# Performance work log

Measured on AMD Instinct MI355X. Metric: run time of the kernel, lower is better.

The kernel has to match this reference:

```python
import jax, jax.numpy as jnp
import numpy as np

WINDOW = (2, 7, 7)
SHIFT = (1, 3, 3)
HEADS = 4


def _rel_pos_index(ws):
    coords = np.stack(np.meshgrid(*[np.arange(w) for w in ws], indexing='ij'))  # (3, wd, wh, ww)
    cf = coords.reshape(3, -1)
    rel = cf[:, :, None] - cf[:, None, :]  # (3, N, N)
    rel = rel.transpose(1, 2, 0).astype(np.int64)
    rel[:, :, 0] += ws[0] - 1
    rel[:, :, 1] += ws[1] - 1
    rel[:, :, 2] += ws[2] - 1
    rel[:, :, 0] *= (2 * ws[1] - 1) * (2 * ws[2] - 1)
    rel[:, :, 1] *= 2 * ws[2] - 1
    return rel.sum(-1)  # (N, N)


def _attn_mask(D, H, W, ws, ss):
    img = np.zeros((1, D, H, W, 1), np.float32)
    cnt = 0
    for d in (slice(None, -ws[0]), slice(-ws[0], -ss[0]), slice(-ss[0], None)):
        for h in (slice(None, -ws[1]), slice(-ws[1], -ss[1]), slice(-ss[1], None)):
            for w in (slice(None, -ws[2]), slice(-ws[2], -ss[2]), slice(-ss[2], None)):
                img[:, d, h, w, :] = cnt
                cnt += 1
    N = ws[0] * ws[1] * ws[2]
    mw = img.reshape(1, D // ws[0], ws[0], H // ws[1], ws[1], W // ws[2], ws[2], 1)
    mw = mw.transpose(0, 1, 3, 5, 2, 4, 6, 7).reshape(-1, N)  # (nW, N)
    diff = mw[:, None, :] - mw[:, :, None]
    return np.where(diff != 0, -100.0, 0.0).astype(np.float32)  # (nW, N, N)


def _win_partition(x, ws):
    B, D, H, W, C = x.shape
    x = x.reshape(B, D // ws[0], ws[0], H // ws[1], ws[1], W // ws[2], ws[2], C)
    return x.transpose(0, 1, 3, 5, 2, 4, 6, 7).reshape(-1, ws[0] * ws[1] * ws[2], C)


def _win_reverse(win, ws, B, D, H, W):
    C = win.shape[-1]
    x = win.reshape(B, D // ws[0], H // ws[1], W // ws[2], ws[0], ws[1], ws[2], C)
    return x.transpose(0, 1, 4, 2, 5, 3, 6, 7).reshape(B, D, H, W, C)


def _ln(x, w, b):
    mu = x.mean(-1, keepdims=True)
    var = x.var(-1, keepdims=True)
    return (x - mu) / jnp.sqrt(var + 1e-5) * w + b


def setup_inputs() -> dict:
    key = jax.random.key(0)
    ks = jax.random.split(key, 8)
    B, D, H, W, C = 4, 8, 56, 56, 128
    hidden = 4 * C
    table = (2 * WINDOW[0] - 1) * (2 * WINDOW[1] - 1) * (2 * WINDOW[2] - 1)
    return {
        'x': jax.random.normal(ks[0], (B, D, H, W, C), jnp.float32),
        'norm1_w': jnp.ones((C,), jnp.float32),
        'norm1_b': jnp.zeros((C,), jnp.float32),
        'qkv_w': 0.02 * jax.random.normal(ks[1], (3 * C, C), jnp.float32),
        'qkv_b': jnp.zeros((3 * C,), jnp.float32),
        'rpb': 0.02 * jax.random.normal(ks[2], (table, HEADS), jnp.float32),
        'proj_w': 0.02 * jax.random.normal(ks[3], (C, C), jnp.float32),
        'proj_b': jnp.zeros((C,), jnp.float32),
        'norm2_w': jnp.ones((C,), jnp.float32),
        'norm2_b': jnp.zeros((C,), jnp.float32),
        'fc1_w': 0.02 * jax.random.normal(ks[4], (hidden, C), jnp.float32),
        'fc1_b': jnp.zeros((hidden,), jnp.float32),
        'fc2_w': 0.02 * jax.random.normal(ks[5], (C, hidden), jnp.float32),
        'fc2_b': jnp.zeros((C,), jnp.float32),
    }


def reference(x, norm1_w, norm1_b, qkv_w, qkv_b, rpb, proj_w, proj_b,
              norm2_w, norm2_b, fc1_w, fc1_b, fc2_w, fc2_b):
    B, D, H, W, C = x.shape
    hd = C // HEADS
    scale = hd ** -0.5
    N = WINDOW[0] * WINDOW[1] * WINDOW[2]

    shortcut = x
    y = _ln(x, norm1_w, norm1_b)
    # cyclic shift (SW-MSA)
    y = jnp.roll(y, (-SHIFT[0], -SHIFT[1], -SHIFT[2]), axis=(1, 2, 3))
    win = _win_partition(y, WINDOW)  # (B_, N, C)
    B_ = win.shape[0]

    qkv = win @ qkv_w.T + qkv_b  # (B_, N, 3C)
    qkv = qkv.reshape(B_, N, 3, HEADS, hd).transpose(2, 0, 3, 1, 4)
    q, k, v = qkv[0] * scale, qkv[1], qkv[2]  # (B_, h, N, hd)

    attn = jnp.einsum('bhnd,bhmd->bhnm', q, k)  # (B_, h, N, N)
    rpi = _rel_pos_index(WINDOW)
    bias = rpb[rpi.reshape(-1)].reshape(N, N, HEADS).transpose(2, 0, 1)  # (h, N, N)
    attn = attn + bias[None]

    mask = jnp.asarray(_attn_mask(D, H, W, WINDOW, SHIFT))  # (nW, N, N)
    nW = mask.shape[0]
    attn = attn.reshape(B_ // nW, nW, HEADS, N, N) + mask[None, :, None]
    attn = jax.nn.softmax(attn.reshape(B_, HEADS, N, N), axis=-1)

    out = jnp.einsum('bhnm,bhmd->bhnd', attn, v)
    out = out.transpose(0, 2, 1, 3).reshape(B_, N, C)
    out = out @ proj_w.T + proj_b

    y = _win_reverse(out, WINDOW, B, D, H, W)
    y = jnp.roll(y, SHIFT, axis=(1, 2, 3))  # reverse cyclic shift
    x = shortcut + y

    h = _ln(x, norm2_w, norm2_b)
    h = jax.nn.gelu(h @ fc1_w.T + fc1_b, approximate=False)
    h = h @ fc2_w.T + fc2_b
    return x + h
```

## Files before the change

kernel.cpp:

```cpp
#include <hip/hip_runtime.h>
#include <math.h>

typedef short bf16x8 __attribute__((ext_vector_type(8)));
typedef float f32x4 __attribute__((ext_vector_type(4)));
typedef unsigned short u16;

#define DEVFN static __device__ __forceinline__

DEVFN u16 f2bf(float f) {
  union { float f; unsigned u; } v; v.f = f;
  return (u16)((v.u + 0x7FFFu + ((v.u >> 16) & 1u)) >> 16);
}

DEVFN float bf2f(u16 u) {
  union { unsigned u; float f; } v; v.u = ((unsigned)u) << 16;
  return v.f;
}

DEVFN void gload16(const void* g, void* l) {
  __builtin_amdgcn_global_load_lds(
      (const __attribute__((address_space(1))) void*)g,
      (__attribute__((address_space(3))) void*)l, 16, 0, 0);
}

DEVFN float gelu_fast(float x) {
  float e = __expf(-1.702f * x);
  return x * __builtin_amdgcn_rcpf(1.0f + e);
}

#define TT 100352
#define BWIN 1024

__global__ void convert4_kernel(const float* __restrict__ a, const float* __restrict__ b,
                                const float* __restrict__ c, const float* __restrict__ d,
                                u16* __restrict__ oa, u16* __restrict__ ob,
                                u16* __restrict__ oc, u16* __restrict__ od) {
  int i = blockIdx.x * 256 + threadIdx.x;
  const float* s; u16* o; int off;
  if (i < 49152)       { s = a; o = oa; off = i; }
  else if (i < 65536)  { s = b; o = ob; off = i - 49152; }
  else if (i < 131072) { s = c; o = oc; off = i - 65536; }
  else                 { s = d; o = od; off = i - 131072; }
  o[off] = f2bf(s[off]);
}

__global__ void biasmask_kernel(const float* __restrict__ rpb, float* __restrict__ bm) {
  int idx = blockIdx.x * 256 + threadIdx.x;
  int lane = idx & 63;
  int rem = idx >> 6;
  int nt = rem % 7;  rem /= 7;
  int mt = rem % 7;  rem /= 7;
  int h = rem & 3;
  int pat = rem >> 2;
  int dB = (pat >> 2) & 1, hB = (pat >> 1) & 1, wB = pat & 1;
  int jc = nt * 16 + (lane & 15);
  f32x4 out;
  #pragma unroll
  for (int r = 0; r < 4; ++r) {
    int ic = mt * 16 + (lane >> 4) * 4 + r;
    float v;
    if (jc > 97) v = -30000.f;
    else if (ic > 97) v = 0.f;
    else {
      int di = ic / 49, ri = ic % 49, hi = ri / 7, wi = ri % 7;
      int dj = jc / 49, rj = jc % 49, hj = rj / 7, wj = rj % 7;
      int tidx = (di - dj + 1) * 169 + (hi - hj + 6) * 13 + (wi - wj + 6);
      v = rpb[tidx * 4 + h];
      int ridi = (dB ? (di == 0 ? 1 : 2) * 9 : 0) + (hB ? (hi < 4 ? 1 : 2) * 3 : 0)
               + (wB ? (wi < 4 ? 1 : 2) : 0);
      int ridj = (dB ? (dj == 0 ? 1 : 2) * 9 : 0) + (hB ? (hj < 4 ? 1 : 2) * 3 : 0)
               + (wB ? (wj < 4 ? 1 : 2) : 0);
      if (ridi != ridj) v -= 100.f;
    }
    out[r] = v;
  }
  *(f32x4*)(bm + (size_t)idx * 4) = out;
}

__global__ __launch_bounds__(256) void qkv_kernel(
    const float* __restrict__ x, const float* __restrict__ n1w, const float* __restrict__ n1b,
    const u16* __restrict__ Bw, const float* __restrict__ bias, u16* __restrict__ outp)
{
  __shared__ u16 smem[24576];
  u16* As = smem;
  u16* Bs = smem + 16384;
  const int m0 = blockIdx.x * 128, n0 = blockIdx.y * 128;
  const int t = threadIdx.x;
  const int wid = t >> 6, lane = t & 63;
  const int wr = wid >> 1, wc = wid & 1;
  const int l15 = lane & 15, lhi = lane >> 4;
  const int srow = lane >> 3;
  const int sslot = lane & 7;
  const int gcol = ((sslot ^ srow) << 3);

  {
    const int rowl = t >> 1, half = t & 1;
    const int grow = m0 + rowl;
    int b_ = grow / 98, n = grow % 98;
    int bb = b_ >> 8, widx = b_ & 255;
    int dwv = widx >> 6, hwv = (widx >> 3) & 7, wwv = widx & 7;
    int dd = n / 49, rr = n % 49, hh = rr / 7, wn = rr % 7;
    int d = (dwv * 2 + dd + 1) & 7;
    int hq = hwv * 7 + hh + 3; if (hq >= 56) hq -= 56;
    int wq = wwv * 7 + wn + 3; if (wq >= 56) wq -= 56;
    size_t src = ((size_t)(((bb * 8 + d) * 56 + hq) * 56 + wq)) * 128 + half * 64;
    f32x4 vals[16];
    float s = 0.f, sq = 0.f;
    #pragma unroll
    for (int j = 0; j < 16; ++j) {
      f32x4 v = *(const f32x4*)(x + src + j * 4);
      vals[j] = v;
      s += v[0] + v[1] + v[2] + v[3];
      sq += v[0]*v[0] + v[1]*v[1] + v[2]*v[2] + v[3]*v[3];
    }
    s += __shfl_xor(s, 1, 64);  sq += __shfl_xor(sq, 1, 64);
    float mu = s * (1.0f / 128.0f);
    float var = sq * (1.0f / 128.0f) - mu * mu;
    float rstd = rsqrtf(var + 1e-5f);
    #pragma unroll
    for (int j = 0; j < 8; ++j) {
      int col = half * 64 + j * 8;
      f32x4 wv0 = *(const f32x4*)(n1w + col);
      f32x4 wv1 = *(const f32x4*)(n1w + col + 4);
      f32x4 bv0 = *(const f32x4*)(n1b + col);
      f32x4 bv1 = *(const f32x4*)(n1b + col + 4);
      u16 hb[8];
      #pragma unroll
      for (int e = 0; e < 4; ++e) {
        hb[e]     = f2bf((vals[2*j][e]   - mu) * rstd * wv0[e] + bv0[e]);
        hb[e + 4] = f2bf((vals[2*j+1][e] - mu) * rstd * wv1[e] + bv1[e]);
      }
      *(bf16x8*)(As + rowl * 128 + ((((col >> 3) ^ (rowl & 7))) << 3)) = *(const bf16x8*)hb;
    }
  }

  f32x4 acc[4][4] = {};
  for (int k0 = 0; k0 < 128; k0 += 64) {
    #pragma unroll
    for (int it = 0; it < 4; ++it) {
      const int rbase = it * 32 + wid * 8;
      const int row = rbase + srow;
      gload16(Bw + (size_t)(n0 + row) * 128 + k0 + gcol, Bs + rbase * 64);
    }
    __syncthreads();
    #pragma unroll
    for (int kk = 0; kk < 64; kk += 32) {
      bf16x8 af[4], bfr[4];
      const int cg = ((k0 + kk) >> 3) + lhi;
      const int csw = (kk + lhi * 8) ^ ((l15 & 7) << 3);
      #pragma unroll
      for (int mi = 0; mi < 4; ++mi) {
        int row = wr * 64 + mi * 16 + l15;
        af[mi] = *(const bf16x8*)(As + row * 128 + ((cg ^ (row & 7)) << 3));
      }
      #pragma unroll
      for (int ni = 0; ni < 4; ++ni)
        bfr[ni] = *(const bf16x8*)(Bs + (wc * 64 + ni * 16 + l15) * 64 + csw);
      #pragma unroll
      for (int mi = 0; mi < 4; ++mi)
        #pragma unroll
        for (int ni = 0; ni < 4; ++ni)
          acc[mi][ni] = __builtin_amdgcn_mfma_f32_16x16x32_bf16(af[mi], bfr[ni], acc[mi][ni], 0, 0, 0);
    }
    __syncthreads();
  }
  const float smul = (n0 == 0) ? 0.17677669529663689f : 1.0f;
  #pragma unroll
  for (int mi = 0; mi < 4; ++mi)
    #pragma unroll
    for (int ni = 0; ni < 4; ++ni) {
      int col = wc * 64 + ni * 16 + l15;
      float bcol = bias[n0 + col];
      #pragma unroll
      for (int r = 0; r < 4; ++r) {
        int row = wr * 64 + mi * 16 + lhi * 4 + r;
        float v = (acc[mi][ni][r] + bcol) * smul;
        smem[row * 128 + (((col >> 3) ^ (row & 7)) << 3) + (col & 7)] = f2bf(v);
      }
    }
  __syncthreads();
  const int rsub = t >> 4, sl = t & 15;
  #pragma unroll
  for (int j = 0; j < 8; ++j) {
    int row = j * 16 + rsub;
    int4 val = *(const int4*)(smem + row * 128 + ((sl ^ (row & 7)) << 3));
    *(int4*)(outp + (size_t)(m0 + row) * 384 + n0 + sl * 8) = val;
  }
}

__global__ __launch_bounds__(256) void proj_kernel(
    const u16* __restrict__ A, const u16* __restrict__ Bw,
    const float* __restrict__ bias, const float* __restrict__ res,
    u16* __restrict__ x2out, const float* __restrict__ n2w,
    const float* __restrict__ n2b, u16* __restrict__ h1out)
{
  __shared__ u16 smem[17664];
  u16* As = smem;
  u16* Bs = smem + 8192;
  const int m0 = blockIdx.x * 128;
  const int t = threadIdx.x;
  const int wid = t >> 6, lane = t & 63;
  const int wr = wid >> 1, wc = wid & 1;
  const int l15 = lane & 15, lhi = lane >> 4;
  const int srow = lane >> 3;
  const int sslot = lane & 7;
  const int gcol = ((sslot ^ srow) << 3);
  f32x4 acc[4][4] = {};
  for (int k0 = 0; k0 < 128; k0 += 64) {
    #pragma unroll
    for (int it = 0; it < 4; ++it) {
      const int rbase = it * 32 + wid * 8;
      const int row = rbase + srow;
      gload16(A + (size_t)(m0 + row) * 128 + k0 + gcol, As + rbase * 64);
      gload16(Bw + (size_t)row * 128 + k0 + gcol, Bs + rbase * 64);
    }
    __syncthreads();
    #pragma unroll
    for (int kk = 0; kk < 64; kk += 32) {
      bf16x8 af[4], bfr[4];
      const int csw = (kk + lhi * 8) ^ ((l15 & 7) << 3);
      #pragma unroll
      for (int mi = 0; mi < 4; ++mi) af[mi] = *(const bf16x8*)(As + (wr * 64 + mi * 16 + l15) * 64 + csw);
      #pragma unroll
      for (int ni = 0; ni < 4; ++ni) bfr[ni] = *(const bf16x8*)(Bs + (wc * 64 + ni * 16 + l15) * 64 + csw);
      #pragma unroll
      for (int mi = 0; mi < 4; ++mi)
        #pragma unroll
        for (int ni = 0; ni < 4; ++ni)
          acc[mi][ni] = __builtin_amdgcn_mfma_f32_16x16x32_bf16(af[mi], bfr[ni], acc[mi][ni], 0, 0, 0);
    }
    __syncthreads();
  }
  float* Pk = (float*)smem;
  #pragma unroll
  for (int half = 0; half < 2; ++half) {
    if (wr == half) {
      #pragma unroll
      for (int ni = 0; ni < 4; ++ni) {
        int col = wc * 64 + ni * 16 + l15;
        float bcol = bias[col];
        #pragma unroll
        for (int mi = 0; mi < 4; ++mi)
          #pragma unroll
          for (int r = 0; r < 4; ++r)
            Pk[(mi * 16 + lhi * 4 + r) * 138 + col] = acc[mi][ni][r] + bcol;
      }
    }
    __syncthreads();
    {
      int rowl = t >> 2, q = t & 3;
      int grow = m0 + half * 64 + rowl;
      int b_ = grow / 98, n = grow % 98;
      int bb = b_ >> 8, widx = b_ & 255;
      int dw = widx >> 6, hw = (widx >> 3) & 7, ww = widx & 7;
      int dd = n / 49, rr = n % 49, hh = rr / 7, wn = rr % 7;
      int d = (dw * 2 + dd + 1) & 7;
      int hq = hw * 7 + hh + 3; if (hq >= 56) hq -= 56;
      int wq = ww * 7 + wn + 3; if (wq >= 56) wq -= 56;
      size_t dbase = ((size_t)(((bb * 8 + d) * 56 + hq) * 56 + wq)) * 128;
      f32x4 vals[8];
      float s = 0.f, sq = 0.f;
      #pragma unroll
      for (int j = 0; j < 8; ++j) {
        int col = j * 16 + q * 4;
        f32x4 pv = *(const f32x4*)(Pk + rowl * 138 + col);
        f32x4 rv = *(const f32x4*)(res + dbase + col);
        f32x4 v = pv + rv;
        vals[j] = v;
        s += v[0] + v[1] + v[2] + v[3];
        sq += v[0]*v[0] + v[1]*v[1] + v[2]*v[2] + v[3]*v[3];
      }
      s += __shfl_xor(s, 1, 64);  sq += __shfl_xor(sq, 1, 64);
      s += __shfl_xor(s, 2, 64);  sq += __shfl_xor(sq, 2, 64);
      float mu = s * (1.0f / 128.0f);
      float var = sq * (1.0f / 128.0f) - mu * mu;
      float rstd = rsqrtf(var + 1e-5f);
      #pragma unroll
      for (int j = 0; j < 8; ++j) {
        int col = j * 16 + q * 4;
        f32x4 wv = *(const f32x4*)(n2w + col);
        f32x4 bv = *(const f32x4*)(n2b + col);
        u16 xb[4], hb[4];
        #pragma unroll
        for (int e = 0; e < 4; ++e) {
          xb[e] = f2bf(vals[j][e]);
          hb[e] = f2bf((vals[j][e] - mu) * rstd * wv[e] + bv[e]);
        }
        *(int2*)(x2out + dbase + col) = *(const int2*)xb;
        *(int2*)(h1out + dbase + col) = *(const int2*)hb;
      }
    }
    __syncthreads();
  }
}

__global__ __launch_bounds__(256, 2) void mlp_kernel(
    const u16* __restrict__ A, const u16* __restrict__ W1, const float* __restrict__ b1,
    const u16* __restrict__ W2, const float* __restrict__ b2,
    const u16* __restrict__ res, float* __restrict__ outp)
{
  __shared__ u16 smem[34816];
  u16* W1c = smem;
  u16* W2c = smem + 8192;
  u16* HsA = smem + 24576;
  float* b1s = (float*)(smem + 33792);
  float* Pk = (float*)smem;
  const int m0 = blockIdx.x * 128;
  const int t = threadIdx.x, wid = t >> 6, lane = t & 63;
  const int l15 = lane & 15, lhi = lane >> 4;
  const int srow4 = lane >> 4, sslot16 = lane & 15;
  const int srow8 = lane >> 3, sslot8 = lane & 7;
  u16* hs = HsA + wid * 2304;

  #pragma unroll
  for (int it = 0; it < 4; ++it) {
    int rb1 = it * 16 + wid * 4, r1 = rb1 + srow4;
    gload16(W1 + (size_t)r1 * 128 + ((sslot16 ^ (r1 & 7)) << 3), W1c + rb1 * 128);
    int rb2 = it * 32 + wid * 8, r2 = rb2 + srow8;
    gload16(W2 + (size_t)r2 * 512 + ((sslot8 ^ (r2 & 7)) << 3), W2c + rb2 * 64);
  }
  if (t < 128) *(f32x4*)(b1s + t * 4) = *(const f32x4*)(b1 + t * 4);
  bf16x8 areg[2][4];
  #pragma unroll
  for (int mi = 0; mi < 2; ++mi)
    #pragma unroll
    for (int kg = 0; kg < 4; ++kg)
      areg[mi][kg] = *(const bf16x8*)(A + (size_t)(m0 + wid * 32 + mi * 16 + l15) * 128 + kg * 32 + lhi * 8);

  f32x4 accO[2][8] = {};
  __syncthreads();
  for (int hc = 0; hc < 8; ++hc) {
    const int cur = (hc & 1) * 8192;
    if (hc < 7) {
      const int nxt = ((hc + 1) & 1) * 8192;
      #pragma unroll
      for (int it = 0; it < 4; ++it) {
        int rb2 = it * 32 + wid * 8, r2 = rb2 + srow8;
        gload16(W2 + (size_t)r2 * 512 + (hc + 1) * 64 + ((sslot8 ^ (r2 & 7)) << 3),
                W2c + nxt + rb2 * 64);
      }
    }
    f32x4 accH[2][4] = {};
    #pragma unroll
    for (int kk = 0; kk < 4; ++kk) {
      bf16x8 bw[4];
      #pragma unroll
      for (int ni = 0; ni < 4; ++ni) {
        int row = ni * 16 + l15;
        bw[ni] = *(const bf16x8*)(W1c + row * 128 + (((kk * 4 + lhi) ^ (row & 7)) << 3));
      }
      #pragma unroll
      for (int mi = 0; mi < 2; ++mi)
        #pragma unroll
        for (int ni = 0; ni < 4; ++ni)
          accH[mi][ni] = __builtin_amdgcn_mfma_f32_16x16x32_bf16(areg[mi][kk], bw[ni], accH[mi][ni], 0, 0, 0);
    }
    #pragma unroll
    for (int mi = 0; mi < 2; ++mi)
      #pragma unroll
      for (int ni = 0; ni < 4; ++ni) {
        float bb = b1s[hc * 64 + ni * 16 + l15];
        #pragma unroll
        for (int r = 0; r < 4; ++r) {
          int tokl = mi * 16 + lhi * 4 + r;
          hs[tokl * 72 + ni * 16 + l15] = f2bf(gelu_fast(accH[mi][ni][r] + bb));
        }
      }
    __syncthreads();
    if (hc < 7) {
      #pragma unroll
      for (int it = 0; it < 4; ++it) {
        int rb1 = it * 16 + wid * 4, r1 = rb1 + srow4;
        gload16(W1 + (size_t)((hc + 1) * 64 + r1) * 128 + ((sslot16 ^ (r1 & 7)) << 3),
                W1c + rb1 * 128);
      }
    }
    #pragma unroll
    for (int kk = 0; kk < 2; ++kk) {
      bf16x8 ah[2], bw2[8];
      #pragma unroll
      for (int mi = 0; mi < 2; ++mi)
        ah[mi] = *(const bf16x8*)(hs + (mi * 16 + l15) * 72 + kk * 32 + lhi * 8);
      #pragma unroll
      for (int ni = 0; ni < 8; ++ni) {
        int row = ni * 16 + l15;
        bw2[ni] = *(const bf16x8*)(W2c + cur + row * 64 + (((kk * 4 + lhi) ^ (row & 7)) << 3));
      }
      #pragma unroll
      for (int mi = 0; mi < 2; ++mi)
        #pragma unroll
        for (int ni = 0; ni < 8; ++ni)
          accO[mi][ni] = __builtin_amdgcn_mfma_f32_16x16x32_bf16(ah[mi], bw2[ni], accO[mi][ni], 0, 0, 0);
    }
    __syncthreads();
  }
  #pragma unroll
  for (int half = 0; half < 2; ++half) {
    if ((wid >> 1) == half) {
      #pragma unroll
      for (int ni = 0; ni < 8; ++ni) {
        int col = ni * 16 + l15;
        float bv = b2[col];
        #pragma unroll
        for (int mi = 0; mi < 2; ++mi)
          #pragma unroll
          for (int r = 0; r < 4; ++r) {
            int tokl = (wid & 1) * 32 + mi * 16 + lhi * 4 + r;
            Pk[tokl * 132 + col] = accO[mi][ni][r] + bv;
          }
      }
    }
    __syncthreads();
    #pragma unroll
    for (int p = 0; p < 8; ++p) {
      int idx = p * 256 + t;
      int row = idx >> 5, c = (idx & 31) * 4;
      size_t gtok = (size_t)(m0 + half * 64 + row);
      f32x4 v = *(const f32x4*)(Pk + row * 132 + c);
      short4 rb = *(const short4*)(res + gtok * 128 + c);
      f32x4 rv;
      rv[0] = bf2f((u16)rb.x); rv[1] = bf2f((u16)rb.y);
      rv[2] = bf2f((u16)rb.z); rv[3] = bf2f((u16)rb.w);
      *(f32x4*)(outp + gtok * 128 + c) = v + rv;
    }
    __syncthreads();
  }
}

__global__ __launch_bounds__(64) void attn_kernel(
    const u16* __restrict__ qkv, const float* __restrict__ biasmask,
    u16* __restrict__ out_win)
{
  __shared__ u16 vT[32][136];
  __shared__ u16 P[16][136];
  const int bid = blockIdx.x;
  const int w = bid >> 2, h = bid & 3;
  const int lane = threadIdx.x;
  const int l15 = lane & 15, lhi = lane >> 4;
  const int widx = w & 255;
  const int dw = widx >> 6, hw = (widx >> 3) & 7, ww = widx & 7;
  const int pat = ((dw == 3) ? 4 : 0) | ((hw == 7) ? 2 : 0) | ((ww == 7) ? 1 : 0);
  const float* bmh = biasmask + (size_t)(pat * 4 + h) * (49 * 256);

  for (int f = lane; f < 160; f += 64) {
    int d = f / 5, c = 96 + (f % 5) * 8;
    *(int4*)&vT[d][c] = (int4){0, 0, 0, 0};
  }
  if (lane < 48) {
    int r = lane / 3, c = 112 + (lane % 3) * 8;
    *(int4*)&P[r][c] = (int4){0, 0, 0, 0};
  }
  const size_t base = (size_t)w * 98 * 384;
  for (int f = lane; f < 392; f += 64) {
    int n = f >> 2, c = (f & 3) * 8;
    int4 v = *(const int4*)(qkv + base + (size_t)n * 384 + 256 + h * 32 + c);
    const u16* pv = (const u16*)&v;
    #pragma unroll
    for (int j = 0; j < 8; ++j) vT[c + j][n] = pv[j];
  }
  const size_t obase = (size_t)w * 98 * 128;
  for (int mt = 0; mt < 7; ++mt) {
    int qn = mt * 16 + l15; if (qn > 97) qn = 97;
    bf16x8 aq = *(const bf16x8*)(qkv + base + (size_t)qn * 384 + h * 32 + lhi * 8);
    f32x4 sf[7];
    #pragma unroll
    for (int nt = 0; nt < 7; ++nt) {
      int kn = nt * 16 + l15; if (kn > 97) kn = 97;
      bf16x8 bk = *(const bf16x8*)(qkv + base + (size_t)kn * 384 + 128 + h * 32 + lhi * 8);
      f32x4 z = {0.f, 0.f, 0.f, 0.f};
      sf[nt] = __builtin_amdgcn_mfma_f32_16x16x32_bf16(aq, bk, z, 0, 0, 0);
    }
    float mx[4] = {-1e30f, -1e30f, -1e30f, -1e30f};
    #pragma unroll
    for (int nt = 0; nt < 7; ++nt) {
      f32x4 bm = *(const f32x4*)(bmh + (mt * 7 + nt) * 256 + lane * 4);
      #pragma unroll
      for (int r = 0; r < 4; ++r) {
        float s = sf[nt][r] + bm[r];
        sf[nt][r] = s;
        mx[r] = fmaxf(mx[r], s);
      }
    }
    #pragma unroll
    for (int m = 1; m < 16; m <<= 1)
      #pragma unroll
      for (int r = 0; r < 4; ++r) mx[r] = fmaxf(mx[r], __shfl_xor(mx[r], m, 64));
    float sm[4] = {0.f, 0.f, 0.f, 0.f};
    #pragma unroll
    for (int nt = 0; nt < 7; ++nt)
      #pragma unroll
      for (int r = 0; r < 4; ++r) {
        float p = __expf(sf[nt][r] - mx[r]);
        sf[nt][r] = p;
        sm[r] += p;
      }
    #pragma unroll
    for (int m = 1; m < 16; m <<= 1)
      #pragma unroll
      for (int r = 0; r < 4; ++r) sm[r] += __shfl_xor(sm[r], m, 64);
    float inv[4];
    #pragma unroll
    for (int r = 0; r < 4; ++r) inv[r] = 1.0f / sm[r];
    #pragma unroll
    for (int nt = 0; nt < 7; ++nt)
      #pragma unroll
      for (int r = 0; r < 4; ++r)
        P[lhi * 4 + r][nt * 16 + l15] = f2bf(sf[nt][r] * inv[r]);
    f32x4 o0 = {}, o1 = {};
    #pragma unroll
    for (int ks = 0; ks < 4; ++ks) {
      bf16x8 ap  = *(const bf16x8*)(&P[l15][ks * 32 + lhi * 8]);
      bf16x8 bv0 = *(const bf16x8*)(&vT[l15][ks * 32 + lhi * 8]);
      bf16x8 bv1 = *(const bf16x8*)(&vT[16 + l15][ks * 32 + lhi * 8]);
      o0 = __builtin_amdgcn_mfma_f32_16x16x32_bf16(ap, bv0, o0, 0, 0, 0);
      o1 = __builtin_amdgcn_mfma_f32_16x16x32_bf16(ap, bv1, o1, 0, 0, 0);
    }
    int irow0 = mt * 16 + lhi * 4;
    #pragma unroll
    for (int r = 0; r < 4; ++r) {
      if (irow0 + r < 98) {
        size_t orow = obase + (size_t)(irow0 + r) * 128 + h * 32;
        out_win[orow + l15] = f2bf(o0[r]);
        out_win[orow + 16 + l15] = f2bf(o1[r]);
      }
    }
  }
}

extern "C" void kernel_launch(void* const* d_in, const int* in_sizes, int n_in,
                              void* d_out, int out_size, void* d_ws, size_t ws_size,
                              hipStream_t stream)
{
  const float* x      = (const float*)d_in[0];
  const float* n1w    = (const float*)d_in[1];
  const float* n1b    = (const float*)d_in[2];
  const float* qkv_w  = (const float*)d_in[3];
  const float* qkv_b  = (const float*)d_in[4];
  const float* rpb    = (const float*)d_in[5];
  const float* proj_w = (const float*)d_in[6];
  const float* proj_b = (const float*)d_in[7];
  const float* n2w    = (const float*)d_in[8];
  const float* n2b    = (const float*)d_in[9];
  const float* fc1_w  = (const float*)d_in[10];
  const float* fc1_b  = (const float*)d_in[11];
  const float* fc2_w  = (const float*)d_in[12];
  const float* fc2_b  = (const float*)d_in[13];

  char* p = (char*)d_ws;
  size_t off = 0;
  auto alloc = [&](size_t bytes) { void* r = p + off; off = (off + bytes + 255) & ~(size_t)255; return r; };
  u16*   qkvw_b    = (u16*)alloc(49152 * 2);
  u16*   projw_b   = (u16*)alloc(16384 * 2);
  u16*   fc1w_b    = (u16*)alloc(65536 * 2);
  u16*   fc2w_b    = (u16*)alloc(65536 * 2);
  float* biasmask  = (float*)alloc(8 * 4 * 49 * 256 * 4);
  u16*   y_win     = (u16*)alloc((size_t)TT * 128 * 2);
  u16*   x2        = (u16*)alloc((size_t)TT * 128 * 2);
  u16*   h1        = (u16*)alloc((size_t)TT * 128 * 2);
  u16*   big       = (u16*)alloc((size_t)TT * 384 * 2);
  if (off > ws_size) return;

  convert4_kernel<<<768, 256, 0, stream>>>(qkv_w, proj_w, fc1_w, fc2_w,
                                           qkvw_b, projw_b, fc1w_b, fc2w_b);
  biasmask_kernel<<<392, 256, 0, stream>>>(rpb, biasmask);
  qkv_kernel<<<dim3(TT / 128, 3), 256, 0, stream>>>(x, n1w, n1b, qkvw_b, qkv_b, big);
  attn_kernel<<<BWIN * 4, 64, 0, stream>>>(big, biasmask, y_win);
  proj_kernel<<<TT / 128, 256, 0, stream>>>(y_win, projw_b, proj_b, x, x2, n2w, n2b, h1);
  mlp_kernel<<<TT / 128, 256, 0, stream>>>(h1, fc1w_b, fc1_b, fc2w_b, fc2_b, x2, (float*)d_out);
}
```

Baseline: 206.5 us.

## Split LN1 from QKV GEMM and pass MLP hidden through registers

LayerNorm1 with the shift and window gather moves into its own kernel that writes bf16 windowed tokens. The QKV GEMM then loads its A tile straight into LDS like the weights. Before, every one of the three column blocks recomputed the LN from fp32 input. In the MLP kernel, the fc1 product is computed transposed so the GELU output can be rearranged into fc2 operands with lane shuffles rather than an LDS staging buffer. The smaller LDS footprint allows a launch bound of 3 blocks per CU. The trade-off is an extra kernel launch and a bf16 round trip through global memory, plus more shuffle instructions and register pressure in the MLP.

```diff
diff --git a/kernel.cpp b/kernel.cpp
--- a/kernel.cpp
+++ b/kernel.cpp
@@ -4,6 +4,7 @@
 typedef short bf16x8 __attribute__((ext_vector_type(8)));
 typedef float f32x4 __attribute__((ext_vector_type(4)));
 typedef unsigned short u16;
+typedef unsigned int u32;
 
 #define DEVFN static __device__ __forceinline__
 
@@ -77,13 +78,40 @@
   *(f32x4*)(bm + (size_t)idx * 4) = out;
 }
 
-__global__ __launch_bounds__(256) void qkv_kernel(
-    const float* __restrict__ x, const float* __restrict__ n1w, const float* __restrict__ n1b,
-    const u16* __restrict__ Bw, const float* __restrict__ bias, u16* __restrict__ outp)
+__global__ __launch_bounds__(256) void ln_kernel(const float* __restrict__ x,
+    const float* __restrict__ w, const float* __restrict__ bterm, u16* __restrict__ out)
 {
-  __shared__ u16 smem[24576];
+  int gw = blockIdx.x * 4 + (threadIdx.x >> 6);
+  int lane = threadIdx.x & 63;
+  int b_ = gw / 98, n = gw % 98;
+  int bb = b_ >> 8, widx = b_ & 255;
+  int dw = widx >> 6, hw = (widx >> 3) & 7, ww = widx & 7;
+  int dd = n / 49, rr = n % 49, hh = rr / 7, wn = rr % 7;
+  int d = (dw * 2 + dd + 1) & 7;
+  int h = hw * 7 + hh + 3; if (h >= 56) h -= 56;
+  int wq = ww * 7 + wn + 3; if (wq >= 56) wq -= 56;
+  size_t src = ((size_t)(((bb * 8 + d) * 56 + h) * 56 + wq)) * 128;
+  float2 v = *(const float2*)(x + src + lane * 2);
+  float s = v.x + v.y, q = v.x * v.x + v.y * v.y;
+  #pragma unroll
+  for (int m = 1; m < 64; m <<= 1) { s += __shfl_xor(s, m, 64); q += __shfl_xor(q, m, 64); }
+  float mu = s * (1.0f / 128.0f);
+  float var = q * (1.0f / 128.0f) - mu * mu;
+  float rstd = rsqrtf(var + 1e-5f);
+  int c = lane * 2;
+  float y0 = (v.x - mu) * rstd * w[c] + bterm[c];
+  float y1 = (v.y - mu) * rstd * w[c + 1] + bterm[c + 1];
+  ushort2 o; o.x = f2bf(y0); o.y = f2bf(y1);
+  *(ushort2*)(out + (size_t)gw * 128 + c) = o;
+}
+
+__global__ __launch_bounds__(256) void qkvgemm_kernel(
+    const u16* __restrict__ A, const u16* __restrict__ Bw,
+    const float* __restrict__ bias, u16* __restrict__ outp)
+{
+  __shared__ u16 smem[16384];
   u16* As = smem;
-  u16* Bs = smem + 16384;
+  u16* Bs = smem + 8192;
   const int m0 = blockIdx.x * 128, n0 = blockIdx.y * 128;
   const int t = threadIdx.x;
   const int wid = t >> 6, lane = t & 63;
@@ -92,70 +120,24 @@
   const int srow = lane >> 3;
   const int sslot = lane & 7;
   const int gcol = ((sslot ^ srow) << 3);
-
-  {
-    const int rowl = t >> 1, half = t & 1;
-    const int grow = m0 + rowl;
-    int b_ = grow / 98, n = grow % 98;
-    int bb = b_ >> 8, widx = b_ & 255;
-    int dwv = widx >> 6, hwv = (widx >> 3) & 7, wwv = widx & 7;
-    int dd = n / 49, rr = n % 49, hh = rr / 7, wn = rr % 7;
-    int d = (dwv * 2 + dd + 1) & 7;
-    int hq = hwv * 7 + hh + 3; if (hq >= 56) hq -= 56;
-    int wq = wwv * 7 + wn + 3; if (wq >= 56) wq -= 56;
-    size_t src = ((size_t)(((bb * 8 + d) * 56 + hq) * 56 + wq)) * 128 + half * 64;
-    f32x4 vals[16];
-    float s = 0.f, sq = 0.f;
-    #pragma unroll
-    for (int j = 0; j < 16; ++j) {
-      f32x4 v = *(const f32x4*)(x + src + j * 4);
-      vals[j] = v;
-      s += v[0] + v[1] + v[2] + v[3];
-      sq += v[0]*v[0] + v[1]*v[1] + v[2]*v[2] + v[3]*v[3];
-    }
-    s += __shfl_xor(s, 1, 64);  sq += __shfl_xor(sq, 1, 64);
-    float mu = s * (1.0f / 128.0f);
-    float var = sq * (1.0f / 128.0f) - mu * mu;
-    float rstd = rsqrtf(var + 1e-5f);
-    #pragma unroll
-    for (int j = 0; j < 8; ++j) {
-      int col = half * 64 + j * 8;
-      f32x4 wv0 = *(const f32x4*)(n1w + col);
-      f32x4 wv1 = *(const f32x4*)(n1w + col + 4);
-      f32x4 bv0 = *(const f32x4*)(n1b + col);
-      f32x4 bv1 = *(const f32x4*)(n1b + col + 4);
-      u16 hb[8];
-      #pragma unroll
-      for (int e = 0; e < 4; ++e) {
-        hb[e]     = f2bf((vals[2*j][e]   - mu) * rstd * wv0[e] + bv0[e]);
-        hb[e + 4] = f2bf((vals[2*j+1][e] - mu) * rstd * wv1[e] + bv1[e]);
-      }
-      *(bf16x8*)(As + rowl * 128 + ((((col >> 3) ^ (rowl & 7))) << 3)) = *(const bf16x8*)hb;
-    }
-  }
-
   f32x4 acc[4][4] = {};
   for (int k0 = 0; k0 < 128; k0 += 64) {
     #pragma unroll
     for (int it = 0; it < 4; ++it) {
       const int rbase = it * 32 + wid * 8;
       const int row = rbase + srow;
+      gload16(A + (size_t)(m0 + row) * 128 + k0 + gcol, As + rbase * 64);
       gload16(Bw + (size_t)(n0 + row) * 128 + k0 + gcol, Bs + rbase * 64);
     }
     __syncthreads();
     #pragma unroll
     for (int kk = 0; kk < 64; kk += 32) {
       bf16x8 af[4], bfr[4];
-      const int cg = ((k0 + kk) >> 3) + lhi;
       const int csw = (kk + lhi * 8) ^ ((l15 & 7) << 3);
       #pragma unroll
-      for (int mi = 0; mi < 4; ++mi) {
-        int row = wr * 64 + mi * 16 + l15;
-        af[mi] = *(const bf16x8*)(As + row * 128 + ((cg ^ (row & 7)) << 3));
-      }
-      #pragma unroll
-      for (int ni = 0; ni < 4; ++ni)
-        bfr[ni] = *(const bf16x8*)(Bs + (wc * 64 + ni * 16 + l15) * 64 + csw);
+      for (int mi = 0; mi < 4; ++mi) af[mi] = *(const bf16x8*)(As + (wr * 64 + mi * 16 + l15) * 64 + csw);
+      #pragma unroll
+      for (int ni = 0; ni < 4; ++ni) bfr[ni] = *(const bf16x8*)(Bs + (wc * 64 + ni * 16 + l15) * 64 + csw);
       #pragma unroll
       for (int mi = 0; mi < 4; ++mi)
         #pragma unroll
@@ -294,23 +276,24 @@
   }
 }
 
-__global__ __launch_bounds__(256, 2) void mlp_kernel(
+__global__ __launch_bounds__(256, 3) void mlp_kernel(
     const u16* __restrict__ A, const u16* __restrict__ W1, const float* __restrict__ b1,
     const u16* __restrict__ W2, const float* __restrict__ b2,
     const u16* __restrict__ res, float* __restrict__ outp)
 {
-  __shared__ u16 smem[34816];
+  __shared__ u16 smem[25600];
   u16* W1c = smem;
   u16* W2c = smem + 8192;
-  u16* HsA = smem + 24576;
-  float* b1s = (float*)(smem + 33792);
+  float* b1s = (float*)(smem + 24576);
   float* Pk = (float*)smem;
   const int m0 = blockIdx.x * 128;
   const int t = threadIdx.x, wid = t >> 6, lane = t & 63;
   const int l15 = lane & 15, lhi = lane >> 4;
   const int srow4 = lane >> 4, sslot16 = lane & 15;
   const int srow8 = lane >> 3, sslot8 = lane & 7;
-  u16* hs = HsA + wid * 2304;
+  const int src0 = ((lane & 16) << 1) + l15;
+  const int src1 = src0 + 16;
+  const bool hiSel = (lane & 32) != 0;
 
   #pragma unroll
   for (int it = 0; it < 4; ++it) {
@@ -322,10 +305,10 @@
   if (t < 128) *(f32x4*)(b1s + t * 4) = *(const f32x4*)(b1 + t * 4);
   bf16x8 areg[2][4];
   #pragma unroll
-  for (int mi = 0; mi < 2; ++mi)
+  for (int tt = 0; tt < 2; ++tt)
     #pragma unroll
     for (int kg = 0; kg < 4; ++kg)
-      areg[mi][kg] = *(const bf16x8*)(A + (size_t)(m0 + wid * 32 + mi * 16 + l15) * 128 + kg * 32 + lhi * 8);
+      areg[tt][kg] = *(const bf16x8*)(A + (size_t)(m0 + wid * 32 + tt * 16 + l15) * 128 + kg * 32 + lhi * 8);
 
   f32x4 accO[2][8] = {};
   __syncthreads();
@@ -340,32 +323,35 @@
                 W2c + nxt + rb2 * 64);
       }
     }
-    f32x4 accH[2][4] = {};
-    #pragma unroll
-    for (int kk = 0; kk < 4; ++kk) {
+    f32x4 accHT[4][2] = {};
+    #pragma unroll
+    for (int kg = 0; kg < 4; ++kg) {
       bf16x8 bw[4];
       #pragma unroll
-      for (int ni = 0; ni < 4; ++ni) {
-        int row = ni * 16 + l15;
-        bw[ni] = *(const bf16x8*)(W1c + row * 128 + (((kk * 4 + lhi) ^ (row & 7)) << 3));
-      }
-      #pragma unroll
-      for (int mi = 0; mi < 2; ++mi)
-        #pragma unroll
-        for (int ni = 0; ni < 4; ++ni)
-          accH[mi][ni] = __builtin_amdgcn_mfma_f32_16x16x32_bf16(areg[mi][kk], bw[ni], accH[mi][ni], 0, 0, 0);
-    }
-    #pragma unroll
-    for (int mi = 0; mi < 2; ++mi)
-      #pragma unroll
-      for (int ni = 0; ni < 4; ++ni) {
-        float bb = b1s[hc * 64 + ni * 16 + l15];
-        #pragma unroll
-        for (int r = 0; r < 4; ++r) {
-          int tokl = mi * 16 + lhi * 4 + r;
-          hs[tokl * 72 + ni * 16 + l15] = f2bf(gelu_fast(accH[mi][ni][r] + bb));
-        }
-      }
+      for (int ht = 0; ht < 4; ++ht) {
+        int row = ht * 16 + l15;
+        bw[ht] = *(const bf16x8*)(W1c + row * 128 + (((kg * 4 + lhi) ^ (row & 7)) << 3));
+      }
+      #pragma unroll
+      for (int ht = 0; ht < 4; ++ht)
+        #pragma unroll
+        for (int tt = 0; tt < 2; ++tt)
+          accHT[ht][tt] = __builtin_amdgcn_mfma_f32_16x16x32_bf16(bw[ht], areg[tt][kg], accHT[ht][tt], 0, 0, 0);
+    }
+    u32 h2x[4][2], h2y[4][2];
+    #pragma unroll
+    for (int ht = 0; ht < 4; ++ht) {
+      f32x4 bbv = *(const f32x4*)(b1s + hc * 64 + ht * 16 + (lhi << 2));
+      #pragma unroll
+      for (int tt = 0; tt < 2; ++tt) {
+        float g0 = gelu_fast(accHT[ht][tt][0] + bbv[0]);
+        float g1 = gelu_fast(accHT[ht][tt][1] + bbv[1]);
+        float g2 = gelu_fast(accHT[ht][tt][2] + bbv[2]);
+        float g3 = gelu_fast(accHT[ht][tt][3] + bbv[3]);
+        h2x[ht][tt] = (u32)f2bf(g0) | ((u32)f2bf(g1) << 16);
+        h2y[ht][tt] = (u32)f2bf(g2) | ((u32)f2bf(g3) << 16);
+      }
+    }
     __syncthreads();
     if (hc < 7) {
       #pragma unroll
@@ -377,20 +363,31 @@
     }
     #pragma unroll
     for (int kk = 0; kk < 2; ++kk) {
-      bf16x8 ah[2], bw2[8];
-      #pragma unroll
-      for (int mi = 0; mi < 2; ++mi)
-        ah[mi] = *(const bf16x8*)(hs + (mi * 16 + l15) * 72 + kk * 32 + lhi * 8);
-      #pragma unroll
-      for (int ni = 0; ni < 8; ++ni) {
-        int row = ni * 16 + l15;
-        bw2[ni] = *(const bf16x8*)(W2c + cur + row * 64 + (((kk * 4 + lhi) ^ (row & 7)) << 3));
-      }
-      #pragma unroll
-      for (int mi = 0; mi < 2; ++mi)
-        #pragma unroll
-        for (int ni = 0; ni < 8; ++ni)
-          accO[mi][ni] = __builtin_amdgcn_mfma_f32_16x16x32_bf16(ah[mi], bw2[ni], accO[mi][ni], 0, 0, 0);
+      bf16x8 bw2[8];
+      #pragma unroll
+      for (int no = 0; no < 8; ++no) {
+        int row = no * 16 + l15;
+        bw2[no] = *(const bf16x8*)(W2c + cur + row * 64 + (((kk * 4 + lhi) ^ (row & 7)) << 3));
+      }
+      #pragma unroll
+      for (int tt = 0; tt < 2; ++tt) {
+        u32 ax0 = (u32)__shfl((int)h2x[2 * kk][tt], src0, 64);
+        u32 bx0 = (u32)__shfl((int)h2x[2 * kk + 1][tt], src0, 64);
+        u32 ay0 = (u32)__shfl((int)h2y[2 * kk][tt], src0, 64);
+        u32 by0 = (u32)__shfl((int)h2y[2 * kk + 1][tt], src0, 64);
+        u32 ax1 = (u32)__shfl((int)h2x[2 * kk][tt], src1, 64);
+        u32 bx1 = (u32)__shfl((int)h2x[2 * kk + 1][tt], src1, 64);
+        u32 ay1 = (u32)__shfl((int)h2y[2 * kk][tt], src1, 64);
+        u32 by1 = (u32)__shfl((int)h2y[2 * kk + 1][tt], src1, 64);
+        union { u32 w[4]; bf16x8 v; } U;
+        U.w[0] = hiSel ? bx0 : ax0;
+        U.w[1] = hiSel ? by0 : ay0;
+        U.w[2] = hiSel ? bx1 : ax1;
+        U.w[3] = hiSel ? by1 : ay1;
+        #pragma unroll
+        for (int no = 0; no < 8; ++no)
+          accO[tt][no] = __builtin_amdgcn_mfma_f32_16x16x32_bf16(U.v, bw2[no], accO[tt][no], 0, 0, 0);
+      }
     }
     __syncthreads();
   }
@@ -398,15 +395,15 @@
   for (int half = 0; half < 2; ++half) {
     if ((wid >> 1) == half) {
       #pragma unroll
-      for (int ni = 0; ni < 8; ++ni) {
-        int col = ni * 16 + l15;
+      for (int no = 0; no < 8; ++no) {
+        int col = no * 16 + l15;
         float bv = b2[col];
         #pragma unroll
-        for (int mi = 0; mi < 2; ++mi)
+        for (int tt = 0; tt < 2; ++tt)
           #pragma unroll
           for (int r = 0; r < 4; ++r) {
-            int tokl = (wid & 1) * 32 + mi * 16 + lhi * 4 + r;
-            Pk[tokl * 132 + col] = accO[mi][ni][r] + bv;
+            int tokl = (wid & 1) * 32 + tt * 16 + lhi * 4 + r;
+            Pk[tokl * 132 + col] = accO[tt][no][r] + bv;
           }
       }
     }
@@ -563,7 +560,8 @@
   convert4_kernel<<<768, 256, 0, stream>>>(qkv_w, proj_w, fc1_w, fc2_w,
                                            qkvw_b, projw_b, fc1w_b, fc2w_b);
   biasmask_kernel<<<392, 256, 0, stream>>>(rpb, biasmask);
-  qkv_kernel<<<dim3(TT / 128, 3), 256, 0, stream>>>(x, n1w, n1b, qkvw_b, qkv_b, big);
+  ln_kernel<<<TT / 4, 256, 0, stream>>>(x, n1w, n1b, y_win);
+  qkvgemm_kernel<<<dim3(TT / 128, 3), 256, 0, stream>>>(y_win, qkvw_b, qkv_b, big);
   attn_kernel<<<BWIN * 4, 64, 0, stream>>>(big, biasmask, y_win);
   proj_kernel<<<TT / 128, 256, 0, stream>>>(y_win, projw_b, proj_b, x, x2, n2w, n2b, h1);
   mlp_kernel<<<TT / 128, 256, 0, stream>>>(h1, fc1w_b, fc1_b, fc2w_b, fc2_b, x2, (float*)d_out);
```

New measurement: 225.3 us. +9.1%, slower.

## Split LN1 into separate kernel and move LN2 into MLP prologue

Applied to the files above, without the earlier changes.

LayerNorm1 moves out of the QKV GEMM into a standalone wave-per-token kernel that writes normalized bf16 rows. The GEMM then loads both operands with direct global-to-LDS copies. LayerNorm2 moves from the proj epilogue into the MLP kernel, which reads x2 once and uses it for both the norm and the residual, removing the h1 buffer write and read. The cost is an extra launch and an extra bf16 activation round trip for LN1, and LN2 is now computed from bf16-rounded x2 instead of fp32 values.

```diff
diff --git a/kernel.cpp b/kernel.cpp
--- a/kernel.cpp
+++ b/kernel.cpp
@@ -4,6 +4,7 @@
 typedef short bf16x8 __attribute__((ext_vector_type(8)));
 typedef float f32x4 __attribute__((ext_vector_type(4)));
 typedef unsigned short u16;
+typedef unsigned int u32;
 
 #define DEVFN static __device__ __forceinline__
 
@@ -77,13 +78,40 @@
   *(f32x4*)(bm + (size_t)idx * 4) = out;
 }
 
-__global__ __launch_bounds__(256) void qkv_kernel(
-    const float* __restrict__ x, const float* __restrict__ n1w, const float* __restrict__ n1b,
-    const u16* __restrict__ Bw, const float* __restrict__ bias, u16* __restrict__ outp)
+__global__ __launch_bounds__(256) void ln_kernel(const float* __restrict__ x,
+    const float* __restrict__ w, const float* __restrict__ bterm, u16* __restrict__ out)
 {
-  __shared__ u16 smem[24576];
+  int gw = blockIdx.x * 4 + (threadIdx.x >> 6);
+  int lane = threadIdx.x & 63;
+  int b_ = gw / 98, n = gw % 98;
+  int bb = b_ >> 8, widx = b_ & 255;
+  int dw = widx >> 6, hw = (widx >> 3) & 7, ww = widx & 7;
+  int dd = n / 49, rr = n % 49, hh = rr / 7, wn = rr % 7;
+  int d = (dw * 2 + dd + 1) & 7;
+  int h = hw * 7 + hh + 3; if (h >= 56) h -= 56;
+  int wq = ww * 7 + wn + 3; if (wq >= 56) wq -= 56;
+  size_t src = ((size_t)(((bb * 8 + d) * 56 + h) * 56 + wq)) * 128;
+  float2 v = *(const float2*)(x + src + lane * 2);
+  float s = v.x + v.y, q = v.x * v.x + v.y * v.y;
+  #pragma unroll
+  for (int m = 1; m < 64; m <<= 1) { s += __shfl_xor(s, m, 64); q += __shfl_xor(q, m, 64); }
+  float mu = s * (1.0f / 128.0f);
+  float var = q * (1.0f / 128.0f) - mu * mu;
+  float rstd = rsqrtf(var + 1e-5f);
+  int c = lane * 2;
+  float y0 = (v.x - mu) * rstd * w[c] + bterm[c];
+  float y1 = (v.y - mu) * rstd * w[c + 1] + bterm[c + 1];
+  ushort2 o; o.x = f2bf(y0); o.y = f2bf(y1);
+  *(ushort2*)(out + (size_t)gw * 128 + c) = o;
+}
+
+__global__ __launch_bounds__(256) void qkvgemm_kernel(
+    const u16* __restrict__ A, const u16* __restrict__ Bw,
+    const float* __restrict__ bias, u16* __restrict__ outp)
+{
+  __shared__ u16 smem[16384];
   u16* As = smem;
-  u16* Bs = smem + 16384;
+  u16* Bs = smem + 8192;
   const int m0 = blockIdx.x * 128, n0 = blockIdx.y * 128;
   const int t = threadIdx.x;
   const int wid = t >> 6, lane = t & 63;
@@ -92,70 +120,24 @@
   const int srow = lane >> 3;
   const int sslot = lane & 7;
   const int gcol = ((sslot ^ srow) << 3);
-
-  {
-    const int rowl = t >> 1, half = t & 1;
-    const int grow = m0 + rowl;
-    int b_ = grow / 98, n = grow % 98;
-    int bb = b_ >> 8, widx = b_ & 255;
-    int dwv = widx >> 6, hwv = (widx >> 3) & 7, wwv = widx & 7;
-    int dd = n / 49, rr = n % 49, hh = rr / 7, wn = rr % 7;
-    int d = (dwv * 2 + dd + 1) & 7;
-    int hq = hwv * 7 + hh + 3; if (hq >= 56) hq -= 56;
-    int wq = wwv * 7 + wn + 3; if (wq >= 56) wq -= 56;
-    size_t src = ((size_t)(((bb * 8 + d) * 56 + hq) * 56 + wq)) * 128 + half * 64;
-    f32x4 vals[16];
-    float s = 0.f, sq = 0.f;
-    #pragma unroll
-    for (int j = 0; j < 16; ++j) {
-      f32x4 v = *(const f32x4*)(x + src + j * 4);
-      vals[j] = v;
-      s += v[0] + v[1] + v[2] + v[3];
-      sq += v[0]*v[0] + v[1]*v[1] + v[2]*v[2] + v[3]*v[3];
-    }
-    s += __shfl_xor(s, 1, 64);  sq += __shfl_xor(sq, 1, 64);
-    float mu = s * (1.0f / 128.0f);
-    float var = sq * (1.0f / 128.0f) - mu * mu;
-    float rstd = rsqrtf(var + 1e-5f);
-    #pragma unroll
-    for (int j = 0; j < 8; ++j) {
-      int col = half * 64 + j * 8;
-      f32x4 wv0 = *(const f32x4*)(n1w + col);
-      f32x4 wv1 = *(const f32x4*)(n1w + col + 4);
-      f32x4 bv0 = *(const f32x4*)(n1b + col);
-      f32x4 bv1 = *(const f32x4*)(n1b + col + 4);
-      u16 hb[8];
-      #pragma unroll
-      for (int e = 0; e < 4; ++e) {
-        hb[e]     = f2bf((vals[2*j][e]   - mu) * rstd * wv0[e] + bv0[e]);
-        hb[e + 4] = f2bf((vals[2*j+1][e] - mu) * rstd * wv1[e] + bv1[e]);
-      }
-      *(bf16x8*)(As + rowl * 128 + ((((col >> 3) ^ (rowl & 7))) << 3)) = *(const bf16x8*)hb;
-    }
-  }
-
   f32x4 acc[4][4] = {};
   for (int k0 = 0; k0 < 128; k0 += 64) {
     #pragma unroll
     for (int it = 0; it < 4; ++it) {
       const int rbase = it * 32 + wid * 8;
       const int row = rbase + srow;
+      gload16(A + (size_t)(m0 + row) * 128 + k0 + gcol, As + rbase * 64);
       gload16(Bw + (size_t)(n0 + row) * 128 + k0 + gcol, Bs + rbase * 64);
     }
     __syncthreads();
     #pragma unroll
     for (int kk = 0; kk < 64; kk += 32) {
       bf16x8 af[4], bfr[4];
-      const int cg = ((k0 + kk) >> 3) + lhi;
       const int csw = (kk + lhi * 8) ^ ((l15 & 7) << 3);
       #pragma unroll
-      for (int mi = 0; mi < 4; ++mi) {
-        int row = wr * 64 + mi * 16 + l15;
-        af[mi] = *(const bf16x8*)(As + row * 128 + ((cg ^ (row & 7)) << 3));
-      }
-      #pragma unroll
-      for (int ni = 0; ni < 4; ++ni)
-        bfr[ni] = *(const bf16x8*)(Bs + (wc * 64 + ni * 16 + l15) * 64 + csw);
+      for (int mi = 0; mi < 4; ++mi) af[mi] = *(const bf16x8*)(As + (wr * 64 + mi * 16 + l15) * 64 + csw);
+      #pragma unroll
+      for (int ni = 0; ni < 4; ++ni) bfr[ni] = *(const bf16x8*)(Bs + (wc * 64 + ni * 16 + l15) * 64 + csw);
       #pragma unroll
       for (int mi = 0; mi < 4; ++mi)
         #pragma unroll
@@ -191,8 +173,7 @@
 __global__ __launch_bounds__(256) void proj_kernel(
     const u16* __restrict__ A, const u16* __restrict__ Bw,
     const float* __restrict__ bias, const float* __restrict__ res,
-    u16* __restrict__ x2out, const float* __restrict__ n2w,
-    const float* __restrict__ n2b, u16* __restrict__ h1out)
+    u16* __restrict__ x2out)
 {
   __shared__ u16 smem[17664];
   u16* As = smem;
@@ -258,36 +239,16 @@
       int hq = hw * 7 + hh + 3; if (hq >= 56) hq -= 56;
       int wq = ww * 7 + wn + 3; if (wq >= 56) wq -= 56;
       size_t dbase = ((size_t)(((bb * 8 + d) * 56 + hq) * 56 + wq)) * 128;
-      f32x4 vals[8];
-      float s = 0.f, sq = 0.f;
       #pragma unroll
       for (int j = 0; j < 8; ++j) {
         int col = j * 16 + q * 4;
         f32x4 pv = *(const f32x4*)(Pk + rowl * 138 + col);
         f32x4 rv = *(const f32x4*)(res + dbase + col);
         f32x4 v = pv + rv;
-        vals[j] = v;
-        s += v[0] + v[1] + v[2] + v[3];
-        sq += v[0]*v[0] + v[1]*v[1] + v[2]*v[2] + v[3]*v[3];
-      }
-      s += __shfl_xor(s, 1, 64);  sq += __shfl_xor(sq, 1, 64);
-      s += __shfl_xor(s, 2, 64);  sq += __shfl_xor(sq, 2, 64);
-      float mu = s * (1.0f / 128.0f);
-      float var = sq * (1.0f / 128.0f) - mu * mu;
-      float rstd = rsqrtf(var + 1e-5f);
-      #pragma unroll
-      for (int j = 0; j < 8; ++j) {
-        int col = j * 16 + q * 4;
-        f32x4 wv = *(const f32x4*)(n2w + col);
-        f32x4 bv = *(const f32x4*)(n2b + col);
-        u16 xb[4], hb[4];
-        #pragma unroll
-        for (int e = 0; e < 4; ++e) {
-          xb[e] = f2bf(vals[j][e]);
-          hb[e] = f2bf((vals[j][e] - mu) * rstd * wv[e] + bv[e]);
-        }
+        u16 xb[4];
+        #pragma unroll
+        for (int e = 0; e < 4; ++e) xb[e] = f2bf(v[e]);
         *(int2*)(x2out + dbase + col) = *(const int2*)xb;
-        *(int2*)(h1out + dbase + col) = *(const int2*)hb;
       }
     }
     __syncthreads();
@@ -295,9 +256,10 @@
 }
 
 __global__ __launch_bounds__(256, 2) void mlp_kernel(
-    const u16* __restrict__ A, const u16* __restrict__ W1, const float* __restrict__ b1,
+    const u16* __restrict__ x2, const float* __restrict__ n2w, const float* __restrict__ n2b,
+    const u16* __restrict__ W1, const float* __restrict__ b1,
     const u16* __restrict__ W2, const float* __restrict__ b2,
-    const u16* __restrict__ res, float* __restrict__ outp)
+    float* __restrict__ outp)
 {
   __shared__ u16 smem[34816];
   u16* W1c = smem;
@@ -320,12 +282,53 @@
     gload16(W2 + (size_t)r2 * 512 + ((sslot8 ^ (r2 & 7)) << 3), W2c + rb2 * 64);
   }
   if (t < 128) *(f32x4*)(b1s + t * 4) = *(const f32x4*)(b1 + t * 4);
+
   bf16x8 areg[2][4];
-  #pragma unroll
-  for (int mi = 0; mi < 2; ++mi)
-    #pragma unroll
-    for (int kg = 0; kg < 4; ++kg)
-      areg[mi][kg] = *(const bf16x8*)(A + (size_t)(m0 + wid * 32 + mi * 16 + l15) * 128 + kg * 32 + lhi * 8);
+  {
+    bf16x8 raw[2][4];
+    float sum[2] = {0.f, 0.f}, sq[2] = {0.f, 0.f};
+    #pragma unroll
+    for (int tt = 0; tt < 2; ++tt)
+      #pragma unroll
+      for (int kg = 0; kg < 4; ++kg) {
+        raw[tt][kg] = *(const bf16x8*)(x2 + (size_t)(m0 + wid * 32 + tt * 16 + l15) * 128 + kg * 32 + lhi * 8);
+        #pragma unroll
+        for (int e = 0; e < 8; ++e) {
+          float f = bf2f((u16)raw[tt][kg][e]);
+          sum[tt] += f; sq[tt] += f * f;
+        }
+      }
+    #pragma unroll
+    for (int tt = 0; tt < 2; ++tt) {
+      sum[tt] += __shfl_xor(sum[tt], 16, 64);  sq[tt] += __shfl_xor(sq[tt], 16, 64);
+      sum[tt] += __shfl_xor(sum[tt], 32, 64);  sq[tt] += __shfl_xor(sq[tt], 32, 64);
+    }
+    float mu[2], rstd[2];
+    #pragma unroll
+    for (int tt = 0; tt < 2; ++tt) {
+      mu[tt] = sum[tt] * (1.0f / 128.0f);
+      float var = sq[tt] * (1.0f / 128.0f) - mu[tt] * mu[tt];
+      rstd[tt] = rsqrtf(var + 1e-5f);
+    }
+    #pragma unroll
+    for (int kg = 0; kg < 4; ++kg) {
+      int col = kg * 32 + lhi * 8;
+      f32x4 w0 = *(const f32x4*)(n2w + col);
+      f32x4 w1 = *(const f32x4*)(n2w + col + 4);
+      f32x4 b0 = *(const f32x4*)(n2b + col);
+      f32x4 b1v = *(const f32x4*)(n2b + col + 4);
+      #pragma unroll
+      for (int tt = 0; tt < 2; ++tt) {
+        u16 hb[8];
+        #pragma unroll
+        for (int e = 0; e < 4; ++e) {
+          hb[e]     = f2bf((bf2f((u16)raw[tt][kg][e])     - mu[tt]) * rstd[tt] * w0[e] + b0[e]);
+          hb[e + 4] = f2bf((bf2f((u16)raw[tt][kg][e + 4]) - mu[tt]) * rstd[tt] * w1[e] + b1v[e]);
+        }
+        areg[tt][kg] = *(const bf16x8*)hb;
+      }
+    }
+  }
 
   f32x4 accO[2][8] = {};
   __syncthreads();
@@ -417,7 +420,7 @@
       int row = idx >> 5, c = (idx & 31) * 4;
       size_t gtok = (size_t)(m0 + half * 64 + row);
       f32x4 v = *(const f32x4*)(Pk + row * 132 + c);
-      short4 rb = *(const short4*)(res + gtok * 128 + c);
+      short4 rb = *(const short4*)(x2 + gtok * 128 + c);
       f32x4 rv;
       rv[0] = bf2f((u16)rb.x); rv[1] = bf2f((u16)rb.y);
       rv[2] = bf2f((u16)rb.z); rv[3] = bf2f((u16)rb.w);
@@ -556,15 +559,15 @@
   float* biasmask  = (float*)alloc(8 * 4 * 49 * 256 * 4);
   u16*   y_win     = (u16*)alloc((size_t)TT * 128 * 2);
   u16*   x2        = (u16*)alloc((size_t)TT * 128 * 2);
-  u16*   h1        = (u16*)alloc((size_t)TT * 128 * 2);
   u16*   big       = (u16*)alloc((size_t)TT * 384 * 2);
   if (off > ws_size) return;
 
   convert4_kernel<<<768, 256, 0, stream>>>(qkv_w, proj_w, fc1_w, fc2_w,
                                            qkvw_b, projw_b, fc1w_b, fc2w_b);
   biasmask_kernel<<<392, 256, 0, stream>>>(rpb, biasmask);
-  qkv_kernel<<<dim3(TT / 128, 3), 256, 0, stream>>>(x, n1w, n1b, qkvw_b, qkv_b, big);
+  ln_kernel<<<TT / 4, 256, 0, stream>>>(x, n1w, n1b, y_win);
+  qkvgemm_kernel<<<dim3(TT / 128, 3), 256, 0, stream>>>(y_win, qkvw_b, qkv_b, big);
   attn_kernel<<<BWIN * 4, 64, 0, stream>>>(big, biasmask, y_win);
-  proj_kernel<<<TT / 128, 256, 0, stream>>>(y_win, projw_b, proj_b, x, x2, n2w, n2b, h1);
-  mlp_kernel<<<TT / 128, 256, 0, stream>>>(h1, fc1w_b, fc1_b, fc2w_b, fc2_b, x2, (float*)d_out);
-}
+  proj_kernel<<<TT / 128, 256, 0, stream>>>(y_win, projw_b, proj_b, x, x2);
+  mlp_kernel<<<TT / 128, 256, 0, stream>>>(x2, n2w, n2b, fc1w_b, fc1_b, fc2w_b, fc2_b, (float*)d_out);
+}
```

New measurement: 190.0 us, median of 2. 1.09x faster.
